# Kernel tuning notes

Measured on AMD Instinct MI355X. Metric: run time of the kernel, lower is better.

The kernel has to match this reference:

```python
import jax, jax.numpy as jnp
import numpy as np

SR = 48000
NC = 8      # num_cylinders
NH = 64     # num_harmonics
NB = 32     # num_noisebands
B_, T_ = 2, 65536
TWO_PI = 2.0 * np.pi


def _gumbel_softmax_hard(key, logits, tau=1.0):
    g = jax.random.gumbel(key, logits.shape, dtype=logits.dtype)
    y = jax.nn.softmax((logits + g) / tau)
    hard = jax.nn.one_hot(jnp.argmax(y, axis=-1), logits.shape[-1], dtype=y.dtype)
    return hard + y - jax.lax.stop_gradient(y)  # straight-through (hard=True)


def _resonant_activation(x, min_mag):
    return jnp.sign(x) * (min_mag + (1.0 - min_mag) * jnp.abs(jnp.tanh(x)))


def _format_coefficients(one_hot, fb_gain, refl, lowpass, tau):
    shifted = jnp.roll(one_hot, 1, axis=-1)
    refl = jax.nn.sigmoid(refl) if lowpass else jnp.tanh(refl)
    k1 = _resonant_activation(refl[0], tau)
    k2 = _resonant_activation(refl[1], tau)
    a1 = k1 * (1.0 - k2)
    a2 = jnp.clip(k2, -0.999, 0.999)
    a1_bound = 0.999 - jnp.abs(a2)
    a1 = jnp.clip(a1, -a1_bound, a1_bound)
    g = jax.nn.sigmoid(fb_gain[0]) ** 0.45
    return one_hot * (a1 * g) + shifted * (a2 * g)


def _sample_wise_lpc(x, a):
    # All-pole IIR: y[t] = x[t] - sum_{i=1..P} a[t, i-1] * y[t-i]
    # x: (B,T), a: (B,T,P) -> (B,T). Inherently sequential scan over T.
    B, T = x.shape
    P = a.shape[-1]

    def step(buf, inp):          # buf: (B,P) = [y[t-1], ..., y[t-P]]
        xt, at = inp             # (B,), (B,P)
        yt = xt - jnp.sum(at * buf, axis=-1)
        buf = jnp.concatenate([yt[:, None], buf[:, :-1]], axis=1)
        return buf, yt

    buf0 = jnp.zeros((B, P), x.dtype)
    _, y = jax.lax.scan(step, buf0, (x.T, jnp.transpose(a, (1, 0, 2))))
    return y.T


def _resonator(excitation, delay_param, fb_gain, refl, min_delay, max_delay, lowpass, tau, key):
    # excitation: (B,1,T)
    sel = _gumbel_softmax_hard(key, delay_param)                 # (max-min,)
    coeffs = _format_coefficients(sel, fb_gain, refl, lowpass, tau)
    coeffs = jnp.concatenate([jnp.zeros(min_delay, coeffs.dtype), coeffs])  # (max_delay,)
    x = excitation[:, 0, :]
    B, T = x.shape
    a = jnp.broadcast_to(coeffs[None, None, :], (B, T, max_delay))
    return _sample_wise_lpc(x, a)[:, None, :]


def setup_inputs() -> dict:
    key = jax.random.key(0)
    ks = jax.random.split(key, 16)
    inp = {
        'f0': jax.random.uniform(ks[0], (B_, 1, T_), jnp.float32),
        'harmonic_amplitudes': jax.random.uniform(ks[1], (B_, NC * NH, T_), jnp.float32),
        'harmonic_fm': jax.random.uniform(ks[2], (B_, 1, T_), jnp.float32),
        'cylinder_phase_offsets': jax.random.normal(ks[3], (B_, NC, T_), jnp.float32),
        'cylinder_pulse_shapes': jax.random.uniform(ks[4], (B_, 2 * NC, T_), jnp.float32),
        'noisebank_amplitudes': jax.random.uniform(ks[5], (B_, NB, T_), jnp.float32),
        'noise_pulse_shapes': jax.random.uniform(ks[6], (B_, 2, T_), jnp.float32),
        'noise_pulse_gain': jax.random.uniform(ks[7], (B_, 1, T_), jnp.float32),
        'flow_noise_gain': jax.random.uniform(ks[8], (B_, 1, T_), jnp.float32),
        'noise_bands': jax.random.normal(ks[9], (NB, T_), jnp.float32),
        'delay_a': jax.random.normal(ks[10], (125 - 40,), jnp.float32),
        'fbgain_a': jnp.ones((1,), jnp.float32),
        'refl_a': jax.random.normal(ks[11], (2,), jnp.float32),
        'delay_b': jax.random.normal(ks[12], (125 - 40,), jnp.float32),
        'fbgain_b': jnp.ones((1,), jnp.float32),
        'refl_b': jax.random.normal(ks[13], (2,), jnp.float32),
        'delay_c': jax.random.normal(ks[14], (40 - 32,), jnp.float32),
        'fbgain_c': jnp.ones((1,), jnp.float32),
        'refl_c': jax.random.normal(ks[15], (2,), jnp.float32),
    }
    return inp


def reference(f0, harmonic_amplitudes, harmonic_fm, cylinder_phase_offsets,
              cylinder_pulse_shapes, noisebank_amplitudes, noise_pulse_shapes,
              noise_pulse_gain, flow_noise_gain, noise_bands,
              delay_a, fbgain_a, refl_a, delay_b, fbgain_b, refl_b,
              delay_c, fbgain_c, refl_c):
    B, C, T = cylinder_phase_offsets.shape
    firing_order = jnp.array([0, 4, 3, 7, 5, 2, 6, 1], dtype=f0.dtype)[:NC]
    firing_angles = firing_order / NC * TWO_PI                         # (8,)
    power_cycle_phase = jnp.cumsum(TWO_PI * f0 / SR, axis=-1) * 0.5    # (B,1,T)
    cylinder_phases = (power_cycle_phase + firing_angles[None, :, None]) % TWO_PI  # (B,8,T)

    hp = (cylinder_phases / TWO_PI) ** harmonic_fm                     # (B,8,T)
    hp = hp * TWO_PI
    harm_idx = jnp.arange(1, NH + 1, dtype=hp.dtype)
    osc = -jnp.sin(hp[:, :, None, :] * harm_idx[None, None, :, None])  # (B,8,64,T)
    amps = harmonic_amplitudes.reshape(B, NC, NH, T)
    harmonics = jnp.sum(osc * amps, axis=2)                            # (B,8,T)

    cyl_alpha = cylinder_pulse_shapes[:, :NC, :]
    cyl_beta = cylinder_pulse_shapes[:, NC:, :]
    cyl_env = (1.0 - jnp.exp(-cyl_alpha * cylinder_phases)) * jnp.exp(-cyl_beta * cylinder_phases)
    harmonics = harmonics * cyl_env * 10.0

    # NoiseBank: fixed noise bands weighted per-sample and summed over bands
    noise = jnp.einsum('bnt,nt->bt', noisebank_amplitudes, noise_bands)[:, None, :]  # (B,1,T)

    n_alpha = noise_pulse_shapes[:, 0:1, :]
    n_beta = noise_pulse_shapes[:, 1:2, :]
    noise_phase = power_cycle_phase % TWO_PI
    noise_env = (1.0 - jnp.exp(-n_alpha * noise_phase)) * jnp.exp(-n_beta * noise_phase)
    noise_bursts = noise * noise_env * noise_pulse_gain
    flow_noise = noise * flow_noise_gain * 0.3
    turbulence = harmonics * noise * (noise_pulse_gain + flow_noise_gain) * 0.7
    cylinders = harmonics + noise_bursts + flow_noise + turbulence     # (B,8,T)

    bank_a = jnp.sum(cylinders[:, :4, :], axis=1, keepdims=True)       # (B,1,T)
    bank_b = jnp.sum(cylinders[:, 4:, :], axis=1, keepdims=True)

    ka, kb, kc = jax.random.split(jax.random.key(42), 3)
    res_a = _resonator(bank_a, delay_a, fbgain_a, refl_a, 40, 125, False, 0.0, ka)
    res_b = _resonator(bank_b, delay_b, fbgain_b, refl_b, 40, 125, False, 0.0, kb)
    res_c = _resonator(res_a + res_b, delay_c, fbgain_c, refl_c, 32, 40, True, 0.0, kc)
    return jnp.sum(res_c, axis=1, keepdims=True)                       # (B,1,T)
```

## Files before the change

kernel.cpp:

```cpp
#include <hip/hip_runtime.h>
#include <cstdint>
#include <cstddef>

#define T_ 65536

__device__ __forceinline__ void tf2x32(uint32_t k0, uint32_t k1,
                                       uint32_t& x0, uint32_t& x1) {
  const uint32_t ks[3] = {k0, k1, k0 ^ k1 ^ 0x1BD11BDAu};
  const int R[8] = {13, 15, 26, 6, 17, 29, 16, 24};
  x0 += ks[0]; x1 += ks[1];
#pragma unroll
  for (int i = 0; i < 5; ++i) {
#pragma unroll
    for (int j = 0; j < 4; ++j) {
      const int r = R[(i & 1) * 4 + j];
      x0 += x1;
      x1 = (x1 << r) | (x1 >> (32 - r));
      x1 ^= x0;
    }
    x0 += ks[(i + 1) % 3];
    x1 += ks[(i + 2) % 3] + (uint32_t)(i + 1);
  }
}

__device__ __forceinline__ float gumbel_from_bits(uint32_t b) {
  float u = __uint_as_float((b >> 9) | 0x3f800000u) - 1.0f;
  u = fmaxf(u, 1.17549435e-38f);
  return -logf(-logf(u));
}

__global__ __launch_bounds__(128) void coef_kernel(
    const float* __restrict__ da, const float* __restrict__ fa, const float* __restrict__ ra,
    const float* __restrict__ db, const float* __restrict__ fb, const float* __restrict__ rb,
    const float* __restrict__ dc, const float* __restrict__ fc, const float* __restrict__ rc,
    float* __restrict__ cws) {
  __shared__ float z[128];
  uint32_t keys[3][2];
#pragma unroll
  for (int q = 0; q < 3; ++q) {
    uint32_t x0 = 0u, x1 = (uint32_t)q;
    tf2x32(0u, 42u, x0, x1);
    keys[q][0] = x0; keys[q][1] = x1;
  }
  const float* dl[3] = {da, db, dc};
  const float* fg[3] = {fa, fb, fc};
  const float* rf[3] = {ra, rb, rc};
  const int Ls[3] = {85, 85, 8};
  const int md[3] = {40, 40, 32};
  const int i = threadIdx.x;
  for (int r = 0; r < 3; ++r) {
    const int L = Ls[r];
    z[i] = -3.4e38f;
    __syncthreads();
    if (i < L) {
      uint32_t x0 = 0u, x1 = (uint32_t)i;
      tf2x32(keys[r][0], keys[r][1], x0, x1);
      z[i] = dl[r][i] + gumbel_from_bits(x0 ^ x1);
    }
    __syncthreads();
    if (i == 0) {
      int p = 0; float best = z[0];
      for (int j = 1; j < L; ++j) { float v = z[j]; if (v > best) { best = v; p = j; } }
      const bool lowpass = (r == 2);
      float r0 = rf[r][0], r1 = rf[r][1];
      if (lowpass) { r0 = 1.f / (1.f + expf(-r0)); r1 = 1.f / (1.f + expf(-r1)); }
      else         { r0 = tanhf(r0);               r1 = tanhf(r1); }
      const float k1 = tanhf(r0), k2 = tanhf(r1);
      float a1 = k1 * (1.f - k2);
      const float a2 = fminf(fmaxf(k2, -0.999f), 0.999f);
      const float bnd = 0.999f - fabsf(a2);
      a1 = fminf(fmaxf(a1, -bnd), bnd);
      const float g = powf(1.f / (1.f + expf(-fg[r][0])), 0.45f);
      const int D1 = md[r] + p + 1;
      const int D2 = md[r] + ((p + 1) % L) + 1;
      const float C1 = a1 * g;
      const float C2 = a2 * g;
      float* cw = cws + r * 32;
      const float bin4[5] = {1.f, 4.f, 6.f, 4.f, 1.f};
      const float c1p[5] = {1.f, C1, C1*C1, C1*C1*C1, C1*C1*C1*C1};
      const float c2p[5] = {1.f, C2, C2*C2, C2*C2*C2, C2*C2*C2*C2};
      for (int j = 0; j < 5; ++j) {
        cw[j]     = (float)((4 - j) * D1 + j * D2);
        cw[5 + j] = bin4[j] * c1p[4 - j] * c2p[j];
      }
      const int   fd[9] = {D1, D2, 2*D1, D1+D2, 2*D2, 3*D1, 2*D1+D2, D1+2*D2, 3*D2};
      const float fn[9] = {-C1, -C2, C1*C1, 2.f*C1*C2, C2*C2,
                           -C1*C1*C1, -3.f*C1*C1*C2, -3.f*C1*C2*C2, -C2*C2*C2};
      for (int k = 0; k < 9; ++k) {
        cw[10 + k] = (float)fd[k];
        cw[19 + k] = fn[k];
      }
    }
    __syncthreads();
  }
}

__global__ __launch_bounds__(1024) void pcp_kernel(const float* __restrict__ f0,
                                                   float* __restrict__ pcp) {
  __shared__ double sm[1024];
  const int b = blockIdx.x;
  const int tid = threadIdx.x;
  const float* src = f0 + (size_t)b * T_;
  const int base = tid * 64;
  double loc = 0.0;
  for (int k = 0; k < 64; ++k) {
    loc += 6.283185307179586 * (double)src[base + k] / 48000.0;
  }
  sm[tid] = loc;
  __syncthreads();
  for (int off = 1; off < 1024; off <<= 1) {
    double v = (tid >= off) ? sm[tid - off] : 0.0;
    __syncthreads();
    sm[tid] += v;
    __syncthreads();
  }
  double run = (tid > 0) ? sm[tid - 1] : 0.0;
  float* dst = pcp + (size_t)b * T_;
  for (int k = 0; k < 64; ++k) {
    run += 6.283185307179586 * (double)src[base + k] / 48000.0;
    dst[base + k] = (float)(run * 0.5);
  }
}

__global__ __launch_bounds__(256) void synth_kernel(
    const float* __restrict__ amps,
    const float* __restrict__ fmg,
    const float* __restrict__ cps,
    const float* __restrict__ nba,
    const float* __restrict__ nps,
    const float* __restrict__ npg,
    const float* __restrict__ fng,
    const float* __restrict__ bands,
    const float* __restrict__ pcp,
    float* __restrict__ bank_a, float* __restrict__ bank_b) {
  const float TPF = 6.283185307179586f;
  const int lane = threadIdx.x & 63;
  const int g    = threadIdx.x >> 6;
  const int blk  = blockIdx.x;
  const int b    = blk >> 9;
  const int t    = (blk & 511) * 128 + lane * 2;
  const size_t bt = (size_t)b * T_ + t;

  __shared__ float2 redN[4][64];
  __shared__ float2 redH[4][64];

  const float p0 = pcp[bt], p1 = pcp[bt + 1];
  const float fm0 = fmg[bt], fm1 = fmg[bt + 1];

  float nse0 = 0.f, nse1 = 0.f;
#pragma unroll
  for (int j = 0; j < 8; ++j) {
    const int n = g * 8 + j;
    const float2 a = *(const float2*)(nba + ((size_t)b * 32 + n) * T_ + t);
    const float2 w = *(const float2*)(bands + (size_t)n * T_ + t);
    nse0 += a.x * w.x; nse1 += a.y * w.y;
  }
  redN[g][lane] = make_float2(nse0, nse1);

  const int order[8] = {0, 4, 3, 7, 5, 2, 6, 1};
  float hp0 = 0.f, hp1 = 0.f;
#pragma unroll
  for (int cc = 0; cc < 2; ++cc) {
    const int c = 2 * g + cc;
    const float ang = ((float)order[c] / 8.0f) * TPF;
    float s0 = p0 + ang; if (s0 >= TPF) s0 -= TPF;
    float s1 = p1 + ang; if (s1 >= TPF) s1 -= TPF;
    const float th0 = TPF * powf(s0 / TPF, fm0);
    const float th1 = TPF * powf(s1 / TPF, fm1);
    float sn0, cs0, sn1, cs1;
    sincosf(th0, &sn0, &cs0);
    sincosf(th1, &sn1, &cs1);
    float sp0 = 0.f, sc0 = sn0, sp1 = 0.f, sc1 = sn1;
    const float tc0 = 2.f * cs0, tc1 = 2.f * cs1;
    float acc0 = 0.f, acc1 = 0.f;
    const float* ap = amps + ((size_t)b * 512 + (size_t)c * 64) * T_ + t;
#pragma unroll 4
    for (int h = 0; h < 64; ++h) {
      const float2 a = *(const float2*)(ap + (size_t)h * T_);
      acc0 += a.x * sc0; acc1 += a.y * sc1;
      const float nx0 = tc0 * sc0 - sp0; sp0 = sc0; sc0 = nx0;
      const float nx1 = tc1 * sc1 - sp1; sp1 = sc1; sc1 = nx1;
    }
    const float2 al = *(const float2*)(cps + ((size_t)b * 16 + c) * T_ + t);
    const float2 be = *(const float2*)(cps + ((size_t)b * 16 + 8 + c) * T_ + t);
    const float env0 = (1.f - expf(-al.x * s0)) * expf(-be.x * s0);
    const float env1 = (1.f - expf(-al.y * s1)) * expf(-be.y * s1);
    hp0 += -acc0 * env0 * 10.f;
    hp1 += -acc1 * env1 * 10.f;
  }
  redH[g][lane] = make_float2(hp0, hp1);
  __syncthreads();

  if (g == 0) {
    const float2 n0 = redN[0][lane], n1 = redN[1][lane],
                 n2 = redN[2][lane], n3 = redN[3][lane];
    const float nseA = n0.x + n1.x + n2.x + n3.x;
    const float nseB = n0.y + n1.y + n2.y + n3.y;
    const float2 h0 = redH[0][lane], h1 = redH[1][lane],
                 h2 = redH[2][lane], h3 = redH[3][lane];
    const float ha0 = h0.x + h1.x, ha1 = h0.y + h1.y;
    const float hb0 = h2.x + h3.x, hb1 = h2.y + h3.y;

    const float g0 = npg[bt], g1 = npg[bt + 1];
    const float fl0 = fng[bt], fl1 = fng[bt + 1];
    const float na0 = nps[(size_t)b * 2 * T_ + t],       na1 = nps[(size_t)b * 2 * T_ + t + 1];
    const float nb0 = nps[((size_t)b * 2 + 1) * T_ + t], nb1 = nps[((size_t)b * 2 + 1) * T_ + t + 1];
    float q0 = p0; if (q0 >= TPF) q0 -= TPF;
    float q1 = p1; if (q1 >= TPF) q1 -= TPF;
    const float ne0 = (1.f - expf(-na0 * q0)) * expf(-nb0 * q0);
    const float ne1 = (1.f - expf(-na1 * q1)) * expf(-nb1 * q1);
    const float com0 = nseA * (ne0 * g0 + fl0 * 0.3f);
    const float com1 = nseB * (ne1 * g1 + fl1 * 0.3f);
    const float K0 = nseA * (g0 + fl0) * 0.7f;
    const float K1 = nseB * (g1 + fl1) * 0.7f;
    *(float2*)(bank_a + bt) = make_float2(ha0 * (1.f + K0) + 4.f * com0,
                                          ha1 * (1.f + K1) + 4.f * com1);
    *(float2*)(bank_b + bt) = make_float2(hb0 * (1.f + K0) + 4.f * com0,
                                          hb1 * (1.f + K1) + 4.f * com1);
  }
}

__global__ __launch_bounds__(256) void prep_ab_kernel(
    const float* __restrict__ BA, const float* __restrict__ BB,
    const float* __restrict__ CW, float* __restrict__ XA, float* __restrict__ XB) {
  const int idx = blockIdx.x * 256 + threadIdx.x;
  const int t = idx & (T_ - 1);
  const int s = idx >> 16;
  const int r = s >> 1, b = s & 1;
  const float* xin = (r == 0 ? BA : BB) + (size_t)b * T_;
  float* xout = (r == 0 ? XA : XB) + (size_t)b * T_;
  const float* cw = CW + r * 32;
  float acc = xin[t];
#pragma unroll
  for (int k = 0; k < 9; ++k) {
    const int d = (int)cw[10 + k];
    const float n = cw[19 + k];
    const int tc = t - d;
    const float u = xin[tc >= 0 ? tc : 0];
    acc += (tc >= 0) ? n * u : 0.f;
  }
  xout[t] = acc;
}

__global__ __launch_bounds__(256) void prep_c_kernel(
    const float* __restrict__ RA, const float* __restrict__ RB,
    const float* __restrict__ CW, float* __restrict__ XC) {
  const int idx = blockIdx.x * 256 + threadIdx.x;
  const int t = idx & (T_ - 1);
  const int b = idx >> 16;
  const float* ya = RA + (size_t)b * T_;
  const float* yb = RB + (size_t)b * T_;
  const float* cw = CW + 64;
  float acc = ya[t] + yb[t];
#pragma unroll
  for (int k = 0; k < 9; ++k) {
    const int d = (int)cw[10 + k];
    const float n = cw[19 + k];
    const int tc = t - d;
    const float u = ya[tc >= 0 ? tc : 0] + yb[tc >= 0 ? tc : 0];
    acc += (tc >= 0) ? n * u : 0.f;
  }
  XC[idx] = acc;
}

__device__ __forceinline__ void gld16(const float* g, float* l) {
  __builtin_amdgcn_global_load_lds((const __attribute__((address_space(1))) void*)g,
                                   (__attribute__((address_space(3))) void*)l, 16, 0, 0);
}

__device__ __forceinline__ void poly_scan(const float* __restrict__ x,
                                          float* __restrict__ y,
                                          const float* __restrict__ cf,
                                          float* __restrict__ sm) {
  const int o = threadIdx.x & 63;
  const int e0 = (int)cf[0], e1 = (int)cf[1], e2 = (int)cf[2],
            e3 = (int)cf[3], e4 = (int)cf[4];
  const float fc0 = cf[5], fc1 = cf[6], fc2 = cf[7], fc3 = cf[8], fc4 = cf[9];
  float* ring = sm;
  float* st   = sm + 1024;

#pragma unroll
  for (int i = 0; i < 16; ++i) ring[o + i * 64] = 0.f;

  {
    const float* g = x + (o << 2);
    gld16(g, st); gld16(g + 256, st + 256);
    gld16(g + 512, st + 512); gld16(g + 768, st + 768);
  }

  float a0 = ring[(o - e0) & 1023];
  float a1v = ring[(o - e1) & 1023];
  float a2v = ring[(o - e2) & 1023];
  float a3v = ring[(o - e3) & 1023];
  float a4v = ring[(o - e4) & 1023];
  float b0 = ring[(o + 64 - e0) & 1023];
  float b1v = ring[(o + 64 - e1) & 1023];
  float b2v = ring[(o + 64 - e2) & 1023];
  float b3v = ring[(o + 64 - e3) & 1023];
  float b4v = ring[(o + 64 - e4) & 1023];

  int t = o;
  for (int ph = 0; ph < 64; ++ph) {
    const int q = ph & 1;
    asm volatile("s_waitcnt vmcnt(0)" ::: "memory");
    if (ph < 63) {
      const float* g = x + (ph + 1) * 1024 + (o << 2);
      float* l = st + (q ^ 1) * 1024;
      gld16(g, l); gld16(g + 256, l + 256);
      gld16(g + 512, l + 512); gld16(g + 768, l + 768);
    }
    const float* bq = st + q * 1024;
    float xv0 = bq[o];
    float xv1 = bq[64 + o];
#pragma unroll
    for (int l = 0; l < 16; l += 2) {
      {
        const float s01 = fmaf(fc0, a0, fc1 * a1v);
        const float s23 = fmaf(fc2, a2v, fc3 * a3v);
        const float yv = xv0 + (s01 + fmaf(fc4, a4v, s23));
        ring[t & 1023] = yv;
        y[t] = yv;
        a0  = ring[(t + 128 - e0) & 1023];
        a1v = ring[(t + 128 - e1) & 1023];
        a2v = ring[(t + 128 - e2) & 1023];
        a3v = ring[(t + 128 - e3) & 1023];
        a4v = ring[(t + 128 - e4) & 1023];
        if (l + 2 < 16) xv0 = bq[(l + 2) * 64 + o];
        t += 64;
      }
      {
        const float s01 = fmaf(fc0, b0, fc1 * b1v);
        const float s23 = fmaf(fc2, b2v, fc3 * b3v);
        const float yv = xv1 + (s01 + fmaf(fc4, b4v, s23));
        ring[t & 1023] = yv;
        y[t] = yv;
        b0  = ring[(t + 128 - e0) & 1023];
        b1v = ring[(t + 128 - e1) & 1023];
        b2v = ring[(t + 128 - e2) & 1023];
        b3v = ring[(t + 128 - e3) & 1023];
        b4v = ring[(t + 128 - e4) & 1023];
        if (l + 3 < 16) xv1 = bq[(l + 3) * 64 + o];
        t += 64;
      }
    }
  }
}

__global__ __launch_bounds__(64) void res_ab_kernel(
    const float* __restrict__ XA, const float* __restrict__ XB,
    float* __restrict__ RA, float* __restrict__ RB, const float* __restrict__ CW) {
  __shared__ float sm[3072];
  const int r = blockIdx.x >> 1;
  const int b = blockIdx.x & 1;
  poly_scan((r == 0 ? XA : XB) + (size_t)b * T_,
            (r == 0 ? RA : RB) + (size_t)b * T_, CW + r * 32, sm);
}

__global__ __launch_bounds__(64) void res_c_kernel(
    const float* __restrict__ XC, float* __restrict__ out,
    const float* __restrict__ CW) {
  __shared__ float sm[3072];
  poly_scan(XC + (size_t)blockIdx.x * T_, out + (size_t)blockIdx.x * T_,
            CW + 64, sm);
}

extern "C" void kernel_launch(void* const* d_in, const int* in_sizes, int n_in,
                              void* d_out, int out_size, void* d_ws, size_t ws_size,
                              hipStream_t stream) {
  const float* f0    = (const float*)d_in[0];
  const float* amps  = (const float*)d_in[1];
  const float* fmg   = (const float*)d_in[2];
  const float* cps   = (const float*)d_in[4];
  const float* nba   = (const float*)d_in[5];
  const float* nps   = (const float*)d_in[6];
  const float* npg   = (const float*)d_in[7];
  const float* fng   = (const float*)d_in[8];
  const float* bands = (const float*)d_in[9];
  const float* da  = (const float*)d_in[10];
  const float* fga = (const float*)d_in[11];
  const float* ra  = (const float*)d_in[12];
  const float* db  = (const float*)d_in[13];
  const float* fgb = (const float*)d_in[14];
  const float* rb  = (const float*)d_in[15];
  const float* dc  = (const float*)d_in[16];
  const float* fgc = (const float*)d_in[17];
  const float* rc  = (const float*)d_in[18];
  float* out = (float*)d_out;
  float* ws  = (float*)d_ws;

  float* S0 = ws;
  float* S1 = ws + 131072;
  float* S2 = ws + 262144;
  float* S3 = ws + 393216;
  float* CW = ws + 524288;

  pcp_kernel<<<2, 1024, 0, stream>>>(f0, S0);
  coef_kernel<<<1, 128, 0, stream>>>(da, fga, ra, db, fgb, rb, dc, fgc, rc, CW);
  synth_kernel<<<1024, 256, 0, stream>>>(amps, fmg, cps, nba, nps, npg, fng, bands,
                                         S0, S1, S2);
  prep_ab_kernel<<<1024, 256, 0, stream>>>(S1, S2, CW, S0, S3);
  res_ab_kernel<<<4, 64, 0, stream>>>(S0, S3, S1, S2, CW);
  prep_c_kernel<<<512, 256, 0, stream>>>(S1, S2, CW, S3);
  res_c_kernel<<<2, 64, 0, stream>>>(S3, out, CW);
}
```

Measured before the change: 260.0 us.

## Fuse pcp and coef kernels, widen synth to float4, triple-buffer scan loads

Merges the phase prefix-sum and coefficient kernels into a single three-block launch, which removes one launch. Widens the synth kernel so each thread handles four samples with float4 loads, halving the grid. Changes the sequential resonator scan from double-buffered to triple-buffered global-to-LDS prefetch with a partial vmcnt wait, so the next two segments are in flight while one is consumed. The costs are more LDS, higher register pressure in synth, and fewer blocks to hide latency.

```diff
diff --git a/kernel.cpp b/kernel.cpp
--- a/kernel.cpp
+++ b/kernel.cpp
@@ -29,96 +29,96 @@
   return -logf(-logf(u));
 }
 
-__global__ __launch_bounds__(128) void coef_kernel(
+__global__ __launch_bounds__(1024) void pcp_coef_kernel(
+    const float* __restrict__ f0, float* __restrict__ pcp,
     const float* __restrict__ da, const float* __restrict__ fa, const float* __restrict__ ra,
     const float* __restrict__ db, const float* __restrict__ fb, const float* __restrict__ rb,
     const float* __restrict__ dc, const float* __restrict__ fc, const float* __restrict__ rc,
     float* __restrict__ cws) {
+  __shared__ double sm[1024];
   __shared__ float z[128];
-  uint32_t keys[3][2];
-#pragma unroll
-  for (int q = 0; q < 3; ++q) {
-    uint32_t x0 = 0u, x1 = (uint32_t)q;
-    tf2x32(0u, 42u, x0, x1);
-    keys[q][0] = x0; keys[q][1] = x1;
-  }
-  const float* dl[3] = {da, db, dc};
-  const float* fg[3] = {fa, fb, fc};
-  const float* rf[3] = {ra, rb, rc};
-  const int Ls[3] = {85, 85, 8};
-  const int md[3] = {40, 40, 32};
-  const int i = threadIdx.x;
-  for (int r = 0; r < 3; ++r) {
-    const int L = Ls[r];
-    z[i] = -3.4e38f;
+  if (blockIdx.x < 2) {
+    const int b = blockIdx.x;
+    const int tid = threadIdx.x;
+    const float* src = f0 + (size_t)b * T_;
+    const int base = tid * 64;
+    double loc = 0.0;
+    for (int k = 0; k < 64; ++k) {
+      loc += 6.283185307179586 * (double)src[base + k] / 48000.0;
+    }
+    sm[tid] = loc;
     __syncthreads();
-    if (i < L) {
-      uint32_t x0 = 0u, x1 = (uint32_t)i;
-      tf2x32(keys[r][0], keys[r][1], x0, x1);
-      z[i] = dl[r][i] + gumbel_from_bits(x0 ^ x1);
-    }
-    __syncthreads();
-    if (i == 0) {
-      int p = 0; float best = z[0];
-      for (int j = 1; j < L; ++j) { float v = z[j]; if (v > best) { best = v; p = j; } }
-      const bool lowpass = (r == 2);
-      float r0 = rf[r][0], r1 = rf[r][1];
-      if (lowpass) { r0 = 1.f / (1.f + expf(-r0)); r1 = 1.f / (1.f + expf(-r1)); }
-      else         { r0 = tanhf(r0);               r1 = tanhf(r1); }
-      const float k1 = tanhf(r0), k2 = tanhf(r1);
-      float a1 = k1 * (1.f - k2);
-      const float a2 = fminf(fmaxf(k2, -0.999f), 0.999f);
-      const float bnd = 0.999f - fabsf(a2);
-      a1 = fminf(fmaxf(a1, -bnd), bnd);
-      const float g = powf(1.f / (1.f + expf(-fg[r][0])), 0.45f);
-      const int D1 = md[r] + p + 1;
-      const int D2 = md[r] + ((p + 1) % L) + 1;
-      const float C1 = a1 * g;
-      const float C2 = a2 * g;
-      float* cw = cws + r * 32;
-      const float bin4[5] = {1.f, 4.f, 6.f, 4.f, 1.f};
-      const float c1p[5] = {1.f, C1, C1*C1, C1*C1*C1, C1*C1*C1*C1};
-      const float c2p[5] = {1.f, C2, C2*C2, C2*C2*C2, C2*C2*C2*C2};
-      for (int j = 0; j < 5; ++j) {
-        cw[j]     = (float)((4 - j) * D1 + j * D2);
-        cw[5 + j] = bin4[j] * c1p[4 - j] * c2p[j];
+    for (int off = 1; off < 1024; off <<= 1) {
+      double v = (tid >= off) ? sm[tid - off] : 0.0;
+      __syncthreads();
+      sm[tid] += v;
+      __syncthreads();
+    }
+    double run = (tid > 0) ? sm[tid - 1] : 0.0;
+    float* dst = pcp + (size_t)b * T_;
+    for (int k = 0; k < 64; ++k) {
+      run += 6.283185307179586 * (double)src[base + k] / 48000.0;
+      dst[base + k] = (float)(run * 0.5);
+    }
+  } else {
+    uint32_t keys[3][2];
+#pragma unroll
+    for (int q = 0; q < 3; ++q) {
+      uint32_t x0 = 0u, x1 = (uint32_t)q;
+      tf2x32(0u, 42u, x0, x1);
+      keys[q][0] = x0; keys[q][1] = x1;
+    }
+    const float* dl[3] = {da, db, dc};
+    const float* fg[3] = {fa, fb, fc};
+    const float* rf[3] = {ra, rb, rc};
+    const int Ls[3] = {85, 85, 8};
+    const int md[3] = {40, 40, 32};
+    const int i = threadIdx.x;
+    for (int r = 0; r < 3; ++r) {
+      const int L = Ls[r];
+      if (i < 128) z[i] = -3.4e38f;
+      __syncthreads();
+      if (i < L) {
+        uint32_t x0 = 0u, x1 = (uint32_t)i;
+        tf2x32(keys[r][0], keys[r][1], x0, x1);
+        z[i] = dl[r][i] + gumbel_from_bits(x0 ^ x1);
       }
-      const int   fd[9] = {D1, D2, 2*D1, D1+D2, 2*D2, 3*D1, 2*D1+D2, D1+2*D2, 3*D2};
-      const float fn[9] = {-C1, -C2, C1*C1, 2.f*C1*C2, C2*C2,
-                           -C1*C1*C1, -3.f*C1*C1*C2, -3.f*C1*C2*C2, -C2*C2*C2};
-      for (int k = 0; k < 9; ++k) {
-        cw[10 + k] = (float)fd[k];
-        cw[19 + k] = fn[k];
+      __syncthreads();
+      if (i == 0) {
+        int p = 0; float best = z[0];
+        for (int j = 1; j < L; ++j) { float v = z[j]; if (v > best) { best = v; p = j; } }
+        const bool lowpass = (r == 2);
+        float r0 = rf[r][0], r1 = rf[r][1];
+        if (lowpass) { r0 = 1.f / (1.f + expf(-r0)); r1 = 1.f / (1.f + expf(-r1)); }
+        else         { r0 = tanhf(r0);               r1 = tanhf(r1); }
+        const float k1 = tanhf(r0), k2 = tanhf(r1);
+        float a1 = k1 * (1.f - k2);
+        const float a2 = fminf(fmaxf(k2, -0.999f), 0.999f);
+        const float bnd = 0.999f - fabsf(a2);
+        a1 = fminf(fmaxf(a1, -bnd), bnd);
+        const float g = powf(1.f / (1.f + expf(-fg[r][0])), 0.45f);
+        const int D1 = md[r] + p + 1;
+        const int D2 = md[r] + ((p + 1) % L) + 1;
+        const float C1 = a1 * g;
+        const float C2 = a2 * g;
+        float* cw = cws + r * 32;
+        const float bin4[5] = {1.f, 4.f, 6.f, 4.f, 1.f};
+        const float c1p[5] = {1.f, C1, C1*C1, C1*C1*C1, C1*C1*C1*C1};
+        const float c2p[5] = {1.f, C2, C2*C2, C2*C2*C2, C2*C2*C2*C2};
+        for (int j = 0; j < 5; ++j) {
+          cw[j]     = (float)((4 - j) * D1 + j * D2);
+          cw[5 + j] = bin4[j] * c1p[4 - j] * c2p[j];
+        }
+        const int   fd[9] = {D1, D2, 2*D1, D1+D2, 2*D2, 3*D1, 2*D1+D2, D1+2*D2, 3*D2};
+        const float fn[9] = {-C1, -C2, C1*C1, 2.f*C1*C2, C2*C2,
+                             -C1*C1*C1, -3.f*C1*C1*C2, -3.f*C1*C2*C2, -C2*C2*C2};
+        for (int k = 0; k < 9; ++k) {
+          cw[10 + k] = (float)fd[k];
+          cw[19 + k] = fn[k];
+        }
       }
-    }
-    __syncthreads();
-  }
-}
-
-__global__ __launch_bounds__(1024) void pcp_kernel(const float* __restrict__ f0,
-                                                   float* __restrict__ pcp) {
-  __shared__ double sm[1024];
-  const int b = blockIdx.x;
-  const int tid = threadIdx.x;
-  const float* src = f0 + (size_t)b * T_;
-  const int base = tid * 64;
-  double loc = 0.0;
-  for (int k = 0; k < 64; ++k) {
-    loc += 6.283185307179586 * (double)src[base + k] / 48000.0;
-  }
-  sm[tid] = loc;
-  __syncthreads();
-  for (int off = 1; off < 1024; off <<= 1) {
-    double v = (tid >= off) ? sm[tid - off] : 0.0;
-    __syncthreads();
-    sm[tid] += v;
-    __syncthreads();
-  }
-  double run = (tid > 0) ? sm[tid - 1] : 0.0;
-  float* dst = pcp + (size_t)b * T_;
-  for (int k = 0; k < 64; ++k) {
-    run += 6.283185307179586 * (double)src[base + k] / 48000.0;
-    dst[base + k] = (float)(run * 0.5);
+      __syncthreads();
+    }
   }
 }
 
@@ -137,86 +137,88 @@
   const int lane = threadIdx.x & 63;
   const int g    = threadIdx.x >> 6;
   const int blk  = blockIdx.x;
-  const int b    = blk >> 9;
-  const int t    = (blk & 511) * 128 + lane * 2;
+  const int b    = blk >> 8;
+  const int t    = (blk & 255) * 256 + lane * 4;
   const size_t bt = (size_t)b * T_ + t;
 
-  __shared__ float2 redN[4][64];
-  __shared__ float2 redH[4][64];
-
-  const float p0 = pcp[bt], p1 = pcp[bt + 1];
-  const float fm0 = fmg[bt], fm1 = fmg[bt + 1];
-
-  float nse0 = 0.f, nse1 = 0.f;
+  __shared__ float4 redN[4][64];
+  __shared__ float4 redH[4][64];
+
+  const float4 p4 = *(const float4*)(pcp + bt);
+  const float4 f4 = *(const float4*)(fmg + bt);
+
+  float4 nse = make_float4(0.f, 0.f, 0.f, 0.f);
 #pragma unroll
   for (int j = 0; j < 8; ++j) {
     const int n = g * 8 + j;
-    const float2 a = *(const float2*)(nba + ((size_t)b * 32 + n) * T_ + t);
-    const float2 w = *(const float2*)(bands + (size_t)n * T_ + t);
-    nse0 += a.x * w.x; nse1 += a.y * w.y;
-  }
-  redN[g][lane] = make_float2(nse0, nse1);
+    const float4 a = *(const float4*)(nba + ((size_t)b * 32 + n) * T_ + t);
+    const float4 w = *(const float4*)(bands + (size_t)n * T_ + t);
+    nse.x += a.x * w.x; nse.y += a.y * w.y;
+    nse.z += a.z * w.z; nse.w += a.w * w.w;
+  }
+  redN[g][lane] = nse;
 
   const int order[8] = {0, 4, 3, 7, 5, 2, 6, 1};
-  float hp0 = 0.f, hp1 = 0.f;
+  float4 hp = make_float4(0.f, 0.f, 0.f, 0.f);
 #pragma unroll
   for (int cc = 0; cc < 2; ++cc) {
     const int c = 2 * g + cc;
     const float ang = ((float)order[c] / 8.0f) * TPF;
-    float s0 = p0 + ang; if (s0 >= TPF) s0 -= TPF;
-    float s1 = p1 + ang; if (s1 >= TPF) s1 -= TPF;
-    const float th0 = TPF * powf(s0 / TPF, fm0);
-    const float th1 = TPF * powf(s1 / TPF, fm1);
-    float sn0, cs0, sn1, cs1;
-    sincosf(th0, &sn0, &cs0);
-    sincosf(th1, &sn1, &cs1);
-    float sp0 = 0.f, sc0 = sn0, sp1 = 0.f, sc1 = sn1;
-    const float tc0 = 2.f * cs0, tc1 = 2.f * cs1;
-    float acc0 = 0.f, acc1 = 0.f;
+#define SETUP(C_)                                                     \
+    float s##C_ = p4.C_ + ang; if (s##C_ >= TPF) s##C_ -= TPF;        \
+    float sn##C_, cs##C_;                                             \
+    sincosf(TPF * powf(s##C_ / TPF, f4.C_), &sn##C_, &cs##C_);        \
+    float sp##C_ = 0.f, sc##C_ = sn##C_;                              \
+    const float tc##C_ = 2.f * cs##C_;                                \
+    float acc##C_ = 0.f;
+    SETUP(x) SETUP(y) SETUP(z) SETUP(w)
+#undef SETUP
     const float* ap = amps + ((size_t)b * 512 + (size_t)c * 64) * T_ + t;
 #pragma unroll 4
     for (int h = 0; h < 64; ++h) {
-      const float2 a = *(const float2*)(ap + (size_t)h * T_);
-      acc0 += a.x * sc0; acc1 += a.y * sc1;
-      const float nx0 = tc0 * sc0 - sp0; sp0 = sc0; sc0 = nx0;
-      const float nx1 = tc1 * sc1 - sp1; sp1 = sc1; sc1 = nx1;
-    }
-    const float2 al = *(const float2*)(cps + ((size_t)b * 16 + c) * T_ + t);
-    const float2 be = *(const float2*)(cps + ((size_t)b * 16 + 8 + c) * T_ + t);
-    const float env0 = (1.f - expf(-al.x * s0)) * expf(-be.x * s0);
-    const float env1 = (1.f - expf(-al.y * s1)) * expf(-be.y * s1);
-    hp0 += -acc0 * env0 * 10.f;
-    hp1 += -acc1 * env1 * 10.f;
-  }
-  redH[g][lane] = make_float2(hp0, hp1);
+      const float4 a = *(const float4*)(ap + (size_t)h * T_);
+#define HSTEP(C_) {                                                   \
+      acc##C_ += a.C_ * sc##C_;                                       \
+      const float nx = tc##C_ * sc##C_ - sp##C_;                      \
+      sp##C_ = sc##C_; sc##C_ = nx; }
+      HSTEP(x) HSTEP(y) HSTEP(z) HSTEP(w)
+#undef HSTEP
+    }
+    const float4 al = *(const float4*)(cps + ((size_t)b * 16 + c) * T_ + t);
+    const float4 be = *(const float4*)(cps + ((size_t)b * 16 + 8 + c) * T_ + t);
+#define ENVACC(C_) {                                                  \
+      const float env = (1.f - expf(-al.C_ * s##C_)) * expf(-be.C_ * s##C_); \
+      hp.C_ += -acc##C_ * env * 10.f; }
+    ENVACC(x) ENVACC(y) ENVACC(z) ENVACC(w)
+#undef ENVACC
+  }
+  redH[g][lane] = hp;
   __syncthreads();
 
   if (g == 0) {
-    const float2 n0 = redN[0][lane], n1 = redN[1][lane],
-                 n2 = redN[2][lane], n3 = redN[3][lane];
-    const float nseA = n0.x + n1.x + n2.x + n3.x;
-    const float nseB = n0.y + n1.y + n2.y + n3.y;
-    const float2 h0 = redH[0][lane], h1 = redH[1][lane],
-                 h2 = redH[2][lane], h3 = redH[3][lane];
-    const float ha0 = h0.x + h1.x, ha1 = h0.y + h1.y;
-    const float hb0 = h2.x + h3.x, hb1 = h2.y + h3.y;
-
-    const float g0 = npg[bt], g1 = npg[bt + 1];
-    const float fl0 = fng[bt], fl1 = fng[bt + 1];
-    const float na0 = nps[(size_t)b * 2 * T_ + t],       na1 = nps[(size_t)b * 2 * T_ + t + 1];
-    const float nb0 = nps[((size_t)b * 2 + 1) * T_ + t], nb1 = nps[((size_t)b * 2 + 1) * T_ + t + 1];
-    float q0 = p0; if (q0 >= TPF) q0 -= TPF;
-    float q1 = p1; if (q1 >= TPF) q1 -= TPF;
-    const float ne0 = (1.f - expf(-na0 * q0)) * expf(-nb0 * q0);
-    const float ne1 = (1.f - expf(-na1 * q1)) * expf(-nb1 * q1);
-    const float com0 = nseA * (ne0 * g0 + fl0 * 0.3f);
-    const float com1 = nseB * (ne1 * g1 + fl1 * 0.3f);
-    const float K0 = nseA * (g0 + fl0) * 0.7f;
-    const float K1 = nseB * (g1 + fl1) * 0.7f;
-    *(float2*)(bank_a + bt) = make_float2(ha0 * (1.f + K0) + 4.f * com0,
-                                          ha1 * (1.f + K1) + 4.f * com1);
-    *(float2*)(bank_b + bt) = make_float2(hb0 * (1.f + K0) + 4.f * com0,
-                                          hb1 * (1.f + K1) + 4.f * com1);
+    const float4 nA = redN[0][lane], nB = redN[1][lane],
+                 nC = redN[2][lane], nD = redN[3][lane];
+    const float4 hA0 = redH[0][lane], hA1 = redH[1][lane],
+                 hB0 = redH[2][lane], hB1 = redH[3][lane];
+    const float4 g4  = *(const float4*)(npg + bt);
+    const float4 fl4 = *(const float4*)(fng + bt);
+    const float4 na4 = *(const float4*)(nps + (size_t)b * 2 * T_ + t);
+    const float4 nb4 = *(const float4*)(nps + ((size_t)b * 2 + 1) * T_ + t);
+    float4 outA, outB;
+#define FIN(C_) {                                                     \
+    const float nse = nA.C_ + nB.C_ + nC.C_ + nD.C_;                  \
+    const float ha = hA0.C_ + hA1.C_;                                 \
+    const float hb = hB0.C_ + hB1.C_;                                 \
+    float q = p4.C_; if (q >= TPF) q -= TPF;                          \
+    const float ne = (1.f - expf(-na4.C_ * q)) * expf(-nb4.C_ * q);   \
+    const float com = nse * (ne * g4.C_ + fl4.C_ * 0.3f);             \
+    const float K = nse * (g4.C_ + fl4.C_) * 0.7f;                    \
+    outA.C_ = ha * (1.f + K) + 4.f * com;                             \
+    outB.C_ = hb * (1.f + K) + 4.f * com; }
+    FIN(x) FIN(y) FIN(z) FIN(w)
+#undef FIN
+    *(float4*)(bank_a + bt) = outA;
+    *(float4*)(bank_b + bt) = outB;
   }
 }
 
@@ -282,11 +284,14 @@
 #pragma unroll
   for (int i = 0; i < 16; ++i) ring[o + i * 64] = 0.f;
 
-  {
-    const float* g = x + (o << 2);
-    gld16(g, st); gld16(g + 256, st + 256);
-    gld16(g + 512, st + 512); gld16(g + 768, st + 768);
-  }
+#pragma unroll
+  for (int seg = 0; seg < 2; ++seg) {
+    const float* g = x + seg * 1024 + (o << 2);
+    float* l = st + seg * 1024;
+    gld16(g, l); gld16(g + 256, l + 256);
+    gld16(g + 512, l + 512); gld16(g + 768, l + 768);
+  }
+  asm volatile("s_waitcnt vmcnt(4)" ::: "memory");
 
   float a0 = ring[(o - e0) & 1023];
   float a1v = ring[(o - e1) & 1023];
@@ -300,16 +305,17 @@
   float b4v = ring[(o + 64 - e4) & 1023];
 
   int t = o;
+  int bufsel = 0;
   for (int ph = 0; ph < 64; ++ph) {
-    const int q = ph & 1;
-    asm volatile("s_waitcnt vmcnt(0)" ::: "memory");
-    if (ph < 63) {
-      const float* g = x + (ph + 1) * 1024 + (o << 2);
-      float* l = st + (q ^ 1) * 1024;
+    if (ph < 62) {
+      const int seg = ph + 2;
+      const float* g = x + seg * 1024 + (o << 2);
+      float* l = st + (seg - (seg / 3) * 3) * 1024;
       gld16(g, l); gld16(g + 256, l + 256);
       gld16(g + 512, l + 512); gld16(g + 768, l + 768);
     }
-    const float* bq = st + q * 1024;
+    const float* bq = st + bufsel * 1024;
+    bufsel = (bufsel == 2) ? 0 : (bufsel + 1);
     float xv0 = bq[o];
     float xv1 = bq[64 + o];
 #pragma unroll
@@ -343,13 +349,14 @@
         t += 64;
       }
     }
+    asm volatile("s_waitcnt vmcnt(20)" ::: "memory");
   }
 }
 
 __global__ __launch_bounds__(64) void res_ab_kernel(
     const float* __restrict__ XA, const float* __restrict__ XB,
     float* __restrict__ RA, float* __restrict__ RB, const float* __restrict__ CW) {
-  __shared__ float sm[3072];
+  __shared__ float sm[4096];
   const int r = blockIdx.x >> 1;
   const int b = blockIdx.x & 1;
   poly_scan((r == 0 ? XA : XB) + (size_t)b * T_,
@@ -359,7 +366,7 @@
 __global__ __launch_bounds__(64) void res_c_kernel(
     const float* __restrict__ XC, float* __restrict__ out,
     const float* __restrict__ CW) {
-  __shared__ float sm[3072];
+  __shared__ float sm[4096];
   poly_scan(XC + (size_t)blockIdx.x * T_, out + (size_t)blockIdx.x * T_,
             CW + 64, sm);
 }
@@ -394,10 +401,10 @@
   float* S3 = ws + 393216;
   float* CW = ws + 524288;
 
-  pcp_kernel<<<2, 1024, 0, stream>>>(f0, S0);
-  coef_kernel<<<1, 128, 0, stream>>>(da, fga, ra, db, fgb, rb, dc, fgc, rc, CW);
-  synth_kernel<<<1024, 256, 0, stream>>>(amps, fmg, cps, nba, nps, npg, fng, bands,
-                                         S0, S1, S2);
+  pcp_coef_kernel<<<3, 1024, 0, stream>>>(f0, S0, da, fga, ra, db, fgb, rb,
+                                          dc, fgc, rc, CW);
+  synth_kernel<<<512, 256, 0, stream>>>(amps, fmg, cps, nba, nps, npg, fng, bands,
+                                        S0, S1, S2);
   prep_ab_kernel<<<1024, 256, 0, stream>>>(S1, S2, CW, S0, S3);
   res_ab_kernel<<<4, 64, 0, stream>>>(S0, S3, S1, S2, CW);
   prep_c_kernel<<<512, 256, 0, stream>>>(S1, S2, CW, S3);
```

After: 254.8 us. 2.0% less time.
